# Optimization experiments

Measured on AMD Instinct MI355X. Metric: run time of the kernel, lower is better.

## Reference

```python
import jax, jax.numpy as jnp
import numpy as np

NUM_VECTORS = 8192
LATENT_DIM = 256
BETA = 0.25


def setup_inputs() -> dict:
    key = jax.random.key(0)
    k1, k2 = jax.random.split(key)
    z = jax.random.normal(k1, (16, LATENT_DIM, 32, 32), dtype=jnp.float32)
    # nn.Embedding weight initialized uniform(-1/K, 1/K)
    emb_weight = jax.random.uniform(
        k2, (NUM_VECTORS, LATENT_DIM), dtype=jnp.float32,
        minval=-1.0 / NUM_VECTORS, maxval=1.0 / NUM_VECTORS)
    return {"z": z, "emb_weight": emb_weight}


def reference(z, emb_weight):
    # z: [B, C, H, W] -> [B, H, W, C]
    z_bhwc = jnp.transpose(z, (0, 2, 3, 1))
    B, H, W, C = z_bhwc.shape
    z_flat = z_bhwc.reshape(-1, C)  # [N, C]

    # Squared distances: ||z||^2 + ||e||^2 - 2 z.e  -> [N, K]
    d = (jnp.sum(z_flat ** 2, axis=1, keepdims=True)
         + jnp.sum(emb_weight ** 2, axis=1)
         - 2.0 * jnp.einsum('nc,kc->nk', z_flat, emb_weight))
    idx = jnp.argmin(d, axis=1)  # [N]

    z_q = emb_weight[idx].reshape(B, H, W, C)

    sg = jax.lax.stop_gradient
    loss = (jnp.mean((sg(z_q) - z_bhwc) ** 2)
            + BETA * jnp.mean((z_q - sg(z_bhwc)) ** 2))

    # Straight-through estimator
    z_q_st = z_bhwc + sg(z_q - z_bhwc)
    z_q_out = jnp.transpose(z_q_st, (0, 3, 1, 2))  # [B, C, H, W]
    return z_q_out, idx, loss
```

## Files before the change

kernel.cpp:

```cpp
#include <hip/hip_runtime.h>
#include <math.h>

#define NB   16
#define CC   256
#define NPTS 16384
#define KK   8192
#define Z_OUT 4194304

#define WS_ENORM 16448
#define WS_CCNT  24640
#define WS_CIDX  41024
#define CAND_CAP 64
#define LCAP     96
#define MARGIN   4.0e-4f

typedef short v8s __attribute__((ext_vector_type(8)));
typedef float v4f __attribute__((ext_vector_type(4)));

__device__ __forceinline__ void gl_lds16(const void* g, void* l) {
    __builtin_amdgcn_global_load_lds((const __attribute__((address_space(1))) void*)g,
                                     (__attribute__((address_space(3))) void*)l, 16, 0, 0);
}
__device__ __forceinline__ unsigned short f2bf(float f) {
    unsigned int u = __float_as_uint(f);
    return (unsigned short)((u + 0x7FFFu + ((u >> 16) & 1u)) >> 16);
}
__device__ __forceinline__ unsigned fenc(float f) {
    unsigned u = __float_as_uint(f);
    return (u & 0x80000000u) ? ~u : (u | 0x80000000u);
}
__device__ __forceinline__ float fdec(unsigned m) {
    unsigned u = (m & 0x80000000u) ? (m & 0x7fffffffu) : ~m;
    return __uint_as_float(u);
}

__global__ void k_prep_z(const float* __restrict__ z, unsigned short* __restrict__ zb16) {
    __shared__ float ts[64][65];
    const int hw0 = blockIdx.x * 64, c0 = blockIdx.y * 64, b = blockIdx.z;
    const int tid = threadIdx.x;
#pragma unroll
    for (int p = 0; p < 4; ++p) {
        int u = p * 256 + tid;
        int ci = u >> 4, j4 = (u & 15) << 2;
        float4 v = *(const float4*)(z + (size_t)b * 262144 + (size_t)(c0 + ci) * 1024 + hw0 + j4);
        ts[ci][j4 + 0] = v.x; ts[ci][j4 + 1] = v.y; ts[ci][j4 + 2] = v.z; ts[ci][j4 + 3] = v.w;
    }
    __syncthreads();
#pragma unroll
    for (int p = 0; p < 4; ++p) {
        int u = p * 256 + tid;
        int hj = u >> 4, i4 = (u & 15) << 2;
        ushort4 o = make_ushort4(f2bf(ts[i4 + 0][hj]), f2bf(ts[i4 + 1][hj]),
                                 f2bf(ts[i4 + 2][hj]), f2bf(ts[i4 + 3][hj]));
        *(ushort4*)(zb16 + (size_t)(b * 1024 + hw0 + hj) * 256 + c0 + i4) = o;
    }
}

__global__ void k_prep_e(const float* __restrict__ emb, unsigned short* __restrict__ ebf,
                         float* __restrict__ enorm, float* __restrict__ lossAcc) {
    const int w = threadIdx.x >> 6, lane = threadIdx.x & 63;
    const int k = blockIdx.x * 4 + w;
    const int i = k * CC + lane * 4;
    float4 v = *(const float4*)(emb + i);
    *(ushort4*)(ebf + i) = make_ushort4(f2bf(v.x), f2bf(v.y), f2bf(v.z), f2bf(v.w));
    float s = v.x * v.x + v.y * v.y + v.z * v.z + v.w * v.w;
    for (int off = 32; off > 0; off >>= 1) s += __shfl_down(s, off);
    if (lane == 0) enorm[k] = s;
    if (blockIdx.x == 0 && threadIdx.x == 0) lossAcc[0] = 0.0f;
}

__global__ __launch_bounds__(512, 2)
void k_cand(const unsigned short* __restrict__ zb16, const unsigned short* __restrict__ ebf,
            int* __restrict__ candCnt, int* __restrict__ candI) {
    __shared__ short    Bs[8][4][512];
    __shared__ unsigned runmaxU[64];
    __shared__ int      cnt[64];
    __shared__ int      lstK[64][LCAP];
    __shared__ float    lstD[64][LCAP];

    const int tid  = threadIdx.x;
    const int lane = tid & 63;
    const int w    = tid >> 6;
    const int nb   = blockIdx.x << 6;
    const int m16  = lane & 15, q = lane >> 4;

    if (tid < 64) { runmaxU[tid] = 0x007FFFFFu;  cnt[tid] = 0; }

#pragma unroll
    for (int p = 0; p < 4; ++p) {
        const int g8 = p * 8 + w;
        const int cc = g8 >> 2, nt = g8 & 3;
        const unsigned short* g = zb16 + (size_t)(nb + nt * 16 + m16) * 256 + cc * 32 + q * 8;
        gl_lds16(g, &Bs[cc][nt][lane * 8]);
    }

    auto loadA = [&](v8s (&a)[4], int kbr, int cc) {
#pragma unroll
        for (int kt = 0; kt < 4; ++kt)
            a[kt] = *(const v8s*)(ebf + (size_t)(kbr + (kt << 4) + m16) * 256 + (cc << 5) + q * 8);
    };
    auto loadB = [&](v8s (&b)[4], int cc) {
#pragma unroll
        for (int nt = 0; nt < 4; ++nt) b[nt] = *(const v8s*)&Bs[cc][nt][lane * 8];
    };

    v8s aR[4][4];
    v8s bP[4], bN[4];

    const int kb0 = w << 6;
    loadA(aR[0], kb0, 0);
    loadA(aR[1], kb0, 1);
    loadA(aR[2], kb0, 2);
    __syncthreads();
    loadB(bP, 0);

#pragma unroll 1
    for (int s = 0; s < 16; ++s) {
        const int kb  = ((s << 3) + w) << 6;
        const int kbn = (s < 15) ? kb + 512 : kb;
        v4f acc[16];
#pragma unroll
        for (int i = 0; i < 16; ++i) acc[i] = (v4f){0.f, 0.f, 0.f, 0.f};

#pragma unroll
        for (int cc = 0; cc < 8; ++cc) {
            if ((cc & 1) == 0) loadB(bN, (cc + 1) & 7);
            else               loadB(bP, (cc + 1) & 7);
            {
                const int tcc = cc + 3;
                if (tcc < 8) loadA(aR[tcc & 3], kb,  tcc);
                else         loadA(aR[tcc & 3], kbn, tcc - 8);
            }
#pragma unroll
            for (int kt = 0; kt < 4; ++kt)
#pragma unroll
                for (int nt = 0; nt < 4; ++nt)
                    acc[kt * 4 + nt] = __builtin_amdgcn_mfma_f32_16x16x32_bf16(
                        aR[cc & 3][kt], ((cc & 1) ? bN[nt] : bP[nt]),
                        acc[kt * 4 + nt], 0, 0, 0);
        }

        float mx[4];
#pragma unroll
        for (int nt = 0; nt < 4; ++nt) {
            float m = acc[0 * 4 + nt][0];
#pragma unroll
            for (int kt = 0; kt < 4; ++kt)
#pragma unroll
                for (int r = 0; r < 4; ++r) m = fmaxf(m, acc[kt * 4 + nt][r]);
            m = fmaxf(m, __shfl_xor(m, 16));
            m = fmaxf(m, __shfl_xor(m, 32));
            mx[nt] = m;
            if (lane < 16) atomicMax(&runmaxU[nt * 16 + lane], fenc(m));
        }
#pragma unroll
        for (int nt = 0; nt < 4; ++nt) {
            const int nl = nt * 16 + m16;
            const float thr = fmaxf(fdec(runmaxU[nl]), mx[nt]) - MARGIN;
#pragma unroll
            for (int kt = 0; kt < 4; ++kt)
#pragma unroll
                for (int r = 0; r < 4; ++r) {
                    if (acc[kt * 4 + nt][r] >= thr) {
                        int k = kb + (kt << 4) + q * 4 + r;
                        int pos = atomicAdd(&cnt[nl], 1);
                        if (pos < LCAP) { lstK[nl][pos] = k; lstD[nl][pos] = acc[kt * 4 + nt][r]; }
                    }
                }
        }
        if (s == 3 || s == 9) __syncthreads();
    }

    __syncthreads();
    if (tid < 64) {
        const int n = nb + tid;
        const int c = cnt[tid];
        if (c > LCAP) {
            candCnt[n] = KK;
        } else {
            const float thr = fdec(runmaxU[tid]) - MARGIN;
            int kept = 0;
            for (int i = 0; i < c; ++i) {
                if (lstD[tid][i] >= thr) {
                    if (kept < CAND_CAP) candI[(size_t)n * CAND_CAP + kept] = lstK[tid][i];
                    ++kept;
                }
            }
            candCnt[n] = (kept > CAND_CAP) ? KK : kept;
        }
    }
}

__global__ __launch_bounds__(256)
void k_final(const float* __restrict__ z, const float* __restrict__ emb,
             const float* __restrict__ enorm, const int* __restrict__ candCnt,
             const int* __restrict__ candI, float* __restrict__ out,
             float* __restrict__ idxf, float* __restrict__ lossAcc) {
    __shared__ float zl[32][261];
    __shared__ int   kis[32];
    __shared__ float red[256];
    const int bid = blockIdx.x;
    const int b = bid >> 5, hw0 = (bid & 31) << 5;
    const int tid = threadIdx.x;
    const int lane = tid & 63, w = tid >> 6;

#pragma unroll
    for (int p = 0; p < 8; ++p) {
        const int u = p * 256 + tid;
        const int c = u >> 3, j4 = (u & 7) << 2;
        float4 v = *(const float4*)(z + (size_t)b * 262144 + (size_t)c * 1024 + hw0 + j4);
        zl[j4 + 0][c] = v.x; zl[j4 + 1][c] = v.y; zl[j4 + 2][c] = v.z; zl[j4 + 3][c] = v.w;
    }
    __syncthreads();

#pragma unroll 1
    for (int rr = 0; rr < 8; ++rr) {
        const int j = w * 8 + rr;
        const int n = b * 1024 + hw0 + j;
        const float4 zv = *(const float4*)&zl[j][lane * 4];
        float zn = zv.x * zv.x;
        zn = fmaf(zv.y, zv.y, zn); zn = fmaf(zv.z, zv.z, zn); zn = fmaf(zv.w, zv.w, zn);
#pragma unroll
        for (int off = 1; off < 64; off <<= 1) zn += __shfl_xor(zn, off);
        const int cnt = candCnt[n];
        float bd = __builtin_inff();
        int   bk = 0x7fffffff;
        if (cnt <= CAND_CAP) {
#pragma unroll 1
            for (int i = 0; i < cnt; ++i) {
                const int k = candI[(size_t)n * CAND_CAP + i];
                const float4 ev = *(const float4*)(emb + (size_t)k * CC + lane * 4);
                float p = zv.x * ev.x;
                p = fmaf(zv.y, ev.y, p);
                p = fmaf(zv.z, ev.z, p);
                p = fmaf(zv.w, ev.w, p);
#pragma unroll
                for (int off = 1; off < 64; off <<= 1) p += __shfl_xor(p, off);
                const float d = (zn + enorm[k]) - (p + p);
                if (d < bd || (d == bd && k < bk)) { bd = d; bk = k; }
            }
        } else {
#pragma unroll 1
            for (int k = 0; k < KK; ++k) {
                const float4 ev = *(const float4*)(emb + (size_t)k * CC + lane * 4);
                float p = zv.x * ev.x;
                p = fmaf(zv.y, ev.y, p);
                p = fmaf(zv.z, ev.z, p);
                p = fmaf(zv.w, ev.w, p);
#pragma unroll
                for (int off = 1; off < 64; off <<= 1) p += __shfl_xor(p, off);
                const float d = (zn + enorm[k]) - (p + p);
                if (d < bd) { bd = d; bk = k; }
            }
        }
        if (lane == 0) { idxf[n] = (float)bk; kis[j] = bk; }
    }
    __syncthreads();

    const int j  = tid & 31;
    const int cg = tid >> 5;
    const int ki0 = kis[j];
    const float* ep = emb + (size_t)ki0 * CC;
    float ls = 0.0f;
#pragma unroll 4
    for (int c = cg * 32; c < cg * 32 + 32; ++c) {
        float e  = ep[c];
        float zv = zl[j][c];
        out[(size_t)b * 262144 + (size_t)c * 1024 + hw0 + j] = e;
        float df = e - zv;
        ls = fmaf(df, df, ls);
    }
    red[tid] = ls;
    __syncthreads();
    for (int s2 = 128; s2 > 0; s2 >>= 1) {
        if (tid < s2) red[tid] += red[tid + s2];
        __syncthreads();
    }
    if (tid == 0) atomicAdd(lossAcc, red[0]);
}

__global__ void k_loss(const float* __restrict__ lossAcc, float* __restrict__ outLoss) {
    if (threadIdx.x == 0) {
        float m = lossAcc[0] * (1.0f / 4194304.0f);
        outLoss[0] = m + 0.25f * m;
    }
}

extern "C" void kernel_launch(void* const* d_in, const int* in_sizes, int n_in,
                              void* d_out, int out_size, void* d_ws, size_t ws_size,
                              hipStream_t stream) {
    const float* z   = (const float*)d_in[0];
    const float* emb = (const float*)d_in[1];
    float* outf = (float*)d_out;
    float* wsf  = (float*)d_ws;

    float* lossAcc = wsf;
    float* enorm   = wsf + WS_ENORM;
    int*   candCnt = (int*)(wsf + WS_CCNT);
    int*   candI   = (int*)(wsf + WS_CIDX);

    unsigned short* zb16 = (unsigned short*)outf;
    unsigned short* ebf  = (unsigned short*)(outf + 2097152);

    k_prep_e<<<2048, 256, 0, stream>>>(emb, ebf, enorm, lossAcc);
    k_prep_z<<<dim3(16, 4, 16), 256, 0, stream>>>(z, zb16);
    k_cand<<<256, 512, 0, stream>>>(zb16, ebf, candCnt, candI);
    k_final<<<512, 256, 0, stream>>>(z, emb, enorm, candCnt, candI,
                                     outf, outf + Z_OUT, lossAcc);
    k_loss<<<1, 64, 0, stream>>>(lossAcc, outf + Z_OUT + NPTS);
}
```

Baseline: 257.9 us.

## Split codebook across block pairs with 128-point tiles, fuse prep kernels and loss finalize

Each candidate-search block now covers 128 query points and half of the codebook, so each codebook A-fragment loaded from global memory feeds twice as many MFMAs. Candidate lists from the two codebook halves are merged through global atomics on candCnt, which is now zeroed in a single fused prep kernel. The separate loss kernel is replaced by a last-block-done counter in k_final. The cost is doubled accumulator registers and LDS per block, a smaller per-point list capacity, and a cross-block merge in which each half applies only its own running max, so more candidates may be emitted or overflow to the full-search fallback.

```diff
diff --git a/kernel.cpp b/kernel.cpp
--- a/kernel.cpp
+++ b/kernel.cpp
@@ -11,7 +11,7 @@
 #define WS_CCNT  24640
 #define WS_CIDX  41024
 #define CAND_CAP 64
-#define LCAP     96
+#define LCAP     56
 #define MARGIN   4.0e-4f
 
 typedef short v8s __attribute__((ext_vector_type(8)));
@@ -34,62 +34,68 @@
     return __uint_as_float(u);
 }
 
-__global__ void k_prep_z(const float* __restrict__ z, unsigned short* __restrict__ zb16) {
-    __shared__ float ts[64][65];
-    const int hw0 = blockIdx.x * 64, c0 = blockIdx.y * 64, b = blockIdx.z;
+__global__ void k_prep(const float* __restrict__ z, const float* __restrict__ emb,
+                       unsigned short* __restrict__ zb16, unsigned short* __restrict__ ebf,
+                       float* __restrict__ enorm, float* __restrict__ lossAcc,
+                       int* __restrict__ doneCnt, int* __restrict__ candCnt) {
+    const int bid = blockIdx.x;
     const int tid = threadIdx.x;
-#pragma unroll
-    for (int p = 0; p < 4; ++p) {
-        int u = p * 256 + tid;
-        int ci = u >> 4, j4 = (u & 15) << 2;
-        float4 v = *(const float4*)(z + (size_t)b * 262144 + (size_t)(c0 + ci) * 1024 + hw0 + j4);
-        ts[ci][j4 + 0] = v.x; ts[ci][j4 + 1] = v.y; ts[ci][j4 + 2] = v.z; ts[ci][j4 + 3] = v.w;
-    }
-    __syncthreads();
-#pragma unroll
-    for (int p = 0; p < 4; ++p) {
-        int u = p * 256 + tid;
-        int hj = u >> 4, i4 = (u & 15) << 2;
-        ushort4 o = make_ushort4(f2bf(ts[i4 + 0][hj]), f2bf(ts[i4 + 1][hj]),
-                                 f2bf(ts[i4 + 2][hj]), f2bf(ts[i4 + 3][hj]));
-        *(ushort4*)(zb16 + (size_t)(b * 1024 + hw0 + hj) * 256 + c0 + i4) = o;
-    }
-}
-
-__global__ void k_prep_e(const float* __restrict__ emb, unsigned short* __restrict__ ebf,
-                         float* __restrict__ enorm, float* __restrict__ lossAcc) {
-    const int w = threadIdx.x >> 6, lane = threadIdx.x & 63;
-    const int k = blockIdx.x * 4 + w;
-    const int i = k * CC + lane * 4;
-    float4 v = *(const float4*)(emb + i);
-    *(ushort4*)(ebf + i) = make_ushort4(f2bf(v.x), f2bf(v.y), f2bf(v.z), f2bf(v.w));
-    float s = v.x * v.x + v.y * v.y + v.z * v.z + v.w * v.w;
-    for (int off = 32; off > 0; off >>= 1) s += __shfl_down(s, off);
-    if (lane == 0) enorm[k] = s;
-    if (blockIdx.x == 0 && threadIdx.x == 0) lossAcc[0] = 0.0f;
+    if (bid < 2048) {
+        const int w = tid >> 6, lane = tid & 63;
+        const int k = bid * 4 + w;
+        const int i = k * CC + lane * 4;
+        float4 v = *(const float4*)(emb + i);
+        *(ushort4*)(ebf + i) = make_ushort4(f2bf(v.x), f2bf(v.y), f2bf(v.z), f2bf(v.w));
+        float s = v.x * v.x + v.y * v.y + v.z * v.z + v.w * v.w;
+        for (int off = 32; off > 0; off >>= 1) s += __shfl_down(s, off);
+        if (lane == 0) enorm[k] = s;
+        if (bid < 64) candCnt[bid * 256 + tid] = 0;
+        if (bid == 0 && tid == 0) { lossAcc[0] = 0.0f; doneCnt[0] = 0; }
+    } else {
+        __shared__ float ts[64][65];
+        const int b2 = bid - 2048;
+        const int hw0 = (b2 & 15) * 64, c0 = ((b2 >> 4) & 3) * 64, b = b2 >> 6;
+#pragma unroll
+        for (int p = 0; p < 4; ++p) {
+            int u = p * 256 + tid;
+            int ci = u >> 4, j4 = (u & 15) << 2;
+            float4 v = *(const float4*)(z + (size_t)b * 262144 + (size_t)(c0 + ci) * 1024 + hw0 + j4);
+            ts[ci][j4 + 0] = v.x; ts[ci][j4 + 1] = v.y; ts[ci][j4 + 2] = v.z; ts[ci][j4 + 3] = v.w;
+        }
+        __syncthreads();
+#pragma unroll
+        for (int p = 0; p < 4; ++p) {
+            int u = p * 256 + tid;
+            int hj = u >> 4, i4 = (u & 15) << 2;
+            ushort4 o = make_ushort4(f2bf(ts[i4 + 0][hj]), f2bf(ts[i4 + 1][hj]),
+                                     f2bf(ts[i4 + 2][hj]), f2bf(ts[i4 + 3][hj]));
+            *(ushort4*)(zb16 + (size_t)(b * 1024 + hw0 + hj) * 256 + c0 + i4) = o;
+        }
+    }
 }
 
 __global__ __launch_bounds__(512, 2)
 void k_cand(const unsigned short* __restrict__ zb16, const unsigned short* __restrict__ ebf,
             int* __restrict__ candCnt, int* __restrict__ candI) {
-    __shared__ short    Bs[8][4][512];
-    __shared__ unsigned runmaxU[64];
-    __shared__ int      cnt[64];
-    __shared__ int      lstK[64][LCAP];
-    __shared__ float    lstD[64][LCAP];
+    __shared__ short    Bs[8][8][512];
+    __shared__ unsigned runmaxU[128];
+    __shared__ int      cnt[128];
+    __shared__ int      lstK[128][LCAP];
+    __shared__ float    lstD[128][LCAP];
 
     const int tid  = threadIdx.x;
     const int lane = tid & 63;
     const int w    = tid >> 6;
-    const int nb   = blockIdx.x << 6;
+    const int nb   = (blockIdx.x >> 1) << 7;
+    const int kh   = blockIdx.x & 1;
     const int m16  = lane & 15, q = lane >> 4;
 
-    if (tid < 64) { runmaxU[tid] = 0x007FFFFFu;  cnt[tid] = 0; }
-
-#pragma unroll
-    for (int p = 0; p < 4; ++p) {
+    if (tid < 128) { runmaxU[tid] = 0x007FFFFFu;  cnt[tid] = 0; }
+
+#pragma unroll
+    for (int p = 0; p < 8; ++p) {
         const int g8 = p * 8 + w;
-        const int cc = g8 >> 2, nt = g8 & 3;
+        const int cc = g8 >> 3, nt = g8 & 7;
         const unsigned short* g = zb16 + (size_t)(nb + nt * 16 + m16) * 256 + cc * 32 + q * 8;
         gl_lds16(g, &Bs[cc][nt][lane * 8]);
     }
@@ -99,94 +105,90 @@
         for (int kt = 0; kt < 4; ++kt)
             a[kt] = *(const v8s*)(ebf + (size_t)(kbr + (kt << 4) + m16) * 256 + (cc << 5) + q * 8);
     };
-    auto loadB = [&](v8s (&b)[4], int cc) {
-#pragma unroll
-        for (int nt = 0; nt < 4; ++nt) b[nt] = *(const v8s*)&Bs[cc][nt][lane * 8];
-    };
-
-    v8s aR[4][4];
-    v8s bP[4], bN[4];
-
-    const int kb0 = w << 6;
-    loadA(aR[0], kb0, 0);
-    loadA(aR[1], kb0, 1);
-    loadA(aR[2], kb0, 2);
-    __syncthreads();
-    loadB(bP, 0);
+
+    v8s aP[4], aN[4];
+    const int kb0 = (kh << 12) + (w << 6);
+    loadA(aP, kb0, 0);
+    __syncthreads();
 
 #pragma unroll 1
-    for (int s = 0; s < 16; ++s) {
-        const int kb  = ((s << 3) + w) << 6;
-        const int kbn = (s < 15) ? kb + 512 : kb;
-        v4f acc[16];
-#pragma unroll
-        for (int i = 0; i < 16; ++i) acc[i] = (v4f){0.f, 0.f, 0.f, 0.f};
+    for (int s = 0; s < 8; ++s) {
+        const int kb  = (kh << 12) + (((s << 3) + w) << 6);
+        const int kbn = (s < 7) ? kb + 512 : kb;
+        v4f acc[32];
+#pragma unroll
+        for (int i = 0; i < 32; ++i) acc[i] = (v4f){0.f, 0.f, 0.f, 0.f};
 
 #pragma unroll
         for (int cc = 0; cc < 8; ++cc) {
-            if ((cc & 1) == 0) loadB(bN, (cc + 1) & 7);
-            else               loadB(bP, (cc + 1) & 7);
-            {
-                const int tcc = cc + 3;
-                if (tcc < 8) loadA(aR[tcc & 3], kb,  tcc);
-                else         loadA(aR[tcc & 3], kbn, tcc - 8);
+            v8s b[8];
+#pragma unroll
+            for (int nt = 0; nt < 8; ++nt) b[nt] = *(const v8s*)&Bs[cc][nt][lane * 8];
+            if ((cc & 1) == 0) {
+                loadA(aN, kb, cc + 1);
+#pragma unroll
+                for (int kt = 0; kt < 4; ++kt)
+#pragma unroll
+                    for (int nt = 0; nt < 8; ++nt)
+                        acc[kt * 8 + nt] = __builtin_amdgcn_mfma_f32_16x16x32_bf16(
+                            aP[kt], b[nt], acc[kt * 8 + nt], 0, 0, 0);
+            } else {
+                if (cc < 7) loadA(aP, kb, cc + 1);
+                else        loadA(aP, kbn, 0);
+#pragma unroll
+                for (int kt = 0; kt < 4; ++kt)
+#pragma unroll
+                    for (int nt = 0; nt < 8; ++nt)
+                        acc[kt * 8 + nt] = __builtin_amdgcn_mfma_f32_16x16x32_bf16(
+                            aN[kt], b[nt], acc[kt * 8 + nt], 0, 0, 0);
             }
+        }
+
+        float mx[8];
+#pragma unroll
+        for (int nt = 0; nt < 8; ++nt) {
+            float m = acc[nt][0];
 #pragma unroll
             for (int kt = 0; kt < 4; ++kt)
 #pragma unroll
-                for (int nt = 0; nt < 4; ++nt)
-                    acc[kt * 4 + nt] = __builtin_amdgcn_mfma_f32_16x16x32_bf16(
-                        aR[cc & 3][kt], ((cc & 1) ? bN[nt] : bP[nt]),
-                        acc[kt * 4 + nt], 0, 0, 0);
-        }
-
-        float mx[4];
-#pragma unroll
-        for (int nt = 0; nt < 4; ++nt) {
-            float m = acc[0 * 4 + nt][0];
-#pragma unroll
-            for (int kt = 0; kt < 4; ++kt)
-#pragma unroll
-                for (int r = 0; r < 4; ++r) m = fmaxf(m, acc[kt * 4 + nt][r]);
+                for (int r = 0; r < 4; ++r) m = fmaxf(m, acc[kt * 8 + nt][r]);
             m = fmaxf(m, __shfl_xor(m, 16));
             m = fmaxf(m, __shfl_xor(m, 32));
             mx[nt] = m;
             if (lane < 16) atomicMax(&runmaxU[nt * 16 + lane], fenc(m));
         }
 #pragma unroll
-        for (int nt = 0; nt < 4; ++nt) {
+        for (int nt = 0; nt < 8; ++nt) {
             const int nl = nt * 16 + m16;
             const float thr = fmaxf(fdec(runmaxU[nl]), mx[nt]) - MARGIN;
 #pragma unroll
             for (int kt = 0; kt < 4; ++kt)
 #pragma unroll
                 for (int r = 0; r < 4; ++r) {
-                    if (acc[kt * 4 + nt][r] >= thr) {
+                    if (acc[kt * 8 + nt][r] >= thr) {
                         int k = kb + (kt << 4) + q * 4 + r;
                         int pos = atomicAdd(&cnt[nl], 1);
-                        if (pos < LCAP) { lstK[nl][pos] = k; lstD[nl][pos] = acc[kt * 4 + nt][r]; }
+                        if (pos < LCAP) { lstK[nl][pos] = k; lstD[nl][pos] = acc[kt * 8 + nt][r]; }
                     }
                 }
         }
-        if (s == 3 || s == 9) __syncthreads();
-    }
-
-    __syncthreads();
-    if (tid < 64) {
+        if (s == 2 || s == 5) __syncthreads();
+    }
+
+    __syncthreads();
+    if (tid < 128) {
         const int n = nb + tid;
         const int c = cnt[tid];
         if (c > LCAP) {
-            candCnt[n] = KK;
+            atomicAdd(&candCnt[n], KK);
         } else {
             const float thr = fdec(runmaxU[tid]) - MARGIN;
-            int kept = 0;
             for (int i = 0; i < c; ++i) {
                 if (lstD[tid][i] >= thr) {
-                    if (kept < CAND_CAP) candI[(size_t)n * CAND_CAP + kept] = lstK[tid][i];
-                    ++kept;
+                    int pos = atomicAdd(&candCnt[n], 1);
+                    if (pos < CAND_CAP) candI[(size_t)n * CAND_CAP + pos] = lstK[tid][i];
                 }
             }
-            candCnt[n] = (kept > CAND_CAP) ? KK : kept;
         }
     }
 }
@@ -195,7 +197,8 @@
 void k_final(const float* __restrict__ z, const float* __restrict__ emb,
              const float* __restrict__ enorm, const int* __restrict__ candCnt,
              const int* __restrict__ candI, float* __restrict__ out,
-             float* __restrict__ idxf, float* __restrict__ lossAcc) {
+             float* __restrict__ idxf, float* __restrict__ lossAcc,
+             int* __restrict__ doneCnt, float* __restrict__ outLoss) {
     __shared__ float zl[32][261];
     __shared__ int   kis[32];
     __shared__ float red[256];
@@ -276,13 +279,15 @@
         if (tid < s2) red[tid] += red[tid + s2];
         __syncthreads();
     }
-    if (tid == 0) atomicAdd(lossAcc, red[0]);
-}
-
-__global__ void k_loss(const float* __restrict__ lossAcc, float* __restrict__ outLoss) {
-    if (threadIdx.x == 0) {
-        float m = lossAcc[0] * (1.0f / 4194304.0f);
-        outLoss[0] = m + 0.25f * m;
+    if (tid == 0) {
+        atomicAdd(lossAcc, red[0]);
+        __threadfence();
+        int old = atomicAdd(doneCnt, 1);
+        if (old == (int)gridDim.x - 1) {
+            float tot = atomicAdd(lossAcc, 0.0f);
+            float m = tot * (1.0f / 4194304.0f);
+            outLoss[0] = m + 0.25f * m;
+        }
     }
 }
 
@@ -295,6 +300,7 @@
     float* wsf  = (float*)d_ws;
 
     float* lossAcc = wsf;
+    int*   doneCnt = (int*)(wsf + 1);
     float* enorm   = wsf + WS_ENORM;
     int*   candCnt = (int*)(wsf + WS_CCNT);
     int*   candI   = (int*)(wsf + WS_CIDX);
@@ -302,10 +308,9 @@
     unsigned short* zb16 = (unsigned short*)outf;
     unsigned short* ebf  = (unsigned short*)(outf + 2097152);
 
-    k_prep_e<<<2048, 256, 0, stream>>>(emb, ebf, enorm, lossAcc);
-    k_prep_z<<<dim3(16, 4, 16), 256, 0, stream>>>(z, zb16);
+    k_prep<<<3072, 256, 0, stream>>>(z, emb, zb16, ebf, enorm, lossAcc, doneCnt, candCnt);
     k_cand<<<256, 512, 0, stream>>>(zb16, ebf, candCnt, candI);
     k_final<<<512, 256, 0, stream>>>(z, emb, enorm, candCnt, candI,
-                                     outf, outf + Z_OUT, lossAcc);
-    k_loss<<<1, 64, 0, stream>>>(lossAcc, outf + Z_OUT + NPTS);
-}
+                                     outf, outf + Z_OUT, lossAcc, doneCnt,
+                                     outf + Z_OUT + NPTS);
+}
```

After: 269.2 us. 1.04x slower.
